# Kernel tuning notes

Hardware: AMD Instinct MI355X
Metric: run time of the kernel (lower is better)

Reference implementation:

```python
import jax, jax.numpy as jnp
import numpy as np

HID = 1024
INTER = 4096
CLIP = 2.5          # config.clip_init_val; SymQuantizer clips to [-CLIP, CLIP]
W_BITS = 8
IN_BITS = 8
EPS = 1e-12         # BertLayerNorm eps


def sym_quant(x, clip, bits):
    """BiT SymQuantizer (layerwise): clamp, scale by global max-abs, round.
    STE: grads flow only through the clamp (zero outside [-clip, clip])."""
    n = float(2 ** (bits - 1) - 1)
    xc = jnp.clip(x, -clip, clip)
    m = jax.lax.stop_gradient(jnp.max(jnp.abs(xc)))
    s = n / m
    q = jnp.round(xc * s) / s
    return xc + jax.lax.stop_gradient(q - xc)


def setup_inputs() -> dict:
    key = jax.random.key(0)
    k0, k1, k2 = jax.random.split(key, 3)
    B, S = 4, 4096
    hidden_states = jax.random.normal(k0, (B, S, INTER), jnp.float32)
    input_tensor = jax.random.normal(k1, (B, S, HID), jnp.float32)
    W = jax.random.normal(k2, (HID, INTER), jnp.float32) * (1.0 / np.sqrt(INTER))
    b = jnp.zeros((HID,), jnp.float32)
    gamma = jnp.ones((HID,), jnp.float32)
    beta = jnp.zeros((HID,), jnp.float32)
    return {"hidden_states": hidden_states, "input_tensor": input_tensor,
            "W": W, "b": b, "gamma": gamma, "beta": beta}


def reference(hidden_states, input_tensor, W, b, gamma, beta):
    # QuantizeLinear: quantize weight and activation, then F.linear
    Wq = sym_quant(W, CLIP, W_BITS)          # [HID, INTER]
    xq = sym_quant(hidden_states, CLIP, IN_BITS)  # [B, S, INTER]
    h = jnp.einsum('bsi,oi->bso', xq, Wq) + b     # [B, S, HID]
    # dropout(p=0.0 / eval mode) is identity
    y = h + input_tensor
    # BertLayerNorm, eps=1e-12
    mu = jnp.mean(y, axis=-1, keepdims=True)
    var = jnp.mean((y - mu) ** 2, axis=-1, keepdims=True)
    return gamma * (y - mu) / jnp.sqrt(var + EPS) + beta
```

## Files before the change

### kernel.cpp

```cpp
#include <hip/hip_runtime.h>
#include <stdint.h>

#define MTOT  16384
#define KDIM  4096
#define NDIM  1024
#define CLIPV 2.5f

typedef __attribute__((ext_vector_type(4)))  int i32x4;
typedef __attribute__((ext_vector_type(16))) int i32x16;
typedef __attribute__((address_space(3))) void lvoid;
typedef __attribute__((address_space(1))) void gvoid;

#define G2L16(g, l) __builtin_amdgcn_global_load_lds((gvoid*)(g), (lvoid*)(l), 16, 0, 0)

__global__ __launch_bounds__(256) void maxabs_kernel(
    const float4* __restrict__ x, int n4, unsigned* __restrict__ slot) {
  __shared__ float red[4];
  float m = 0.f;
  const int stride = gridDim.x * blockDim.x;
  for (int i = blockIdx.x * blockDim.x + threadIdx.x; i < n4; i += stride) {
    float4 v = x[i];
    m = fmaxf(m, fmaxf(fmaxf(fabsf(v.x), fabsf(v.y)),
                       fmaxf(fabsf(v.z), fabsf(v.w))));
    if (__any(m >= CLIPV)) break;
  }
  m = fminf(m, CLIPV);
#pragma unroll
  for (int off = 32; off > 0; off >>= 1) m = fmaxf(m, __shfl_xor(m, off));
  if ((threadIdx.x & 63) == 0) red[threadIdx.x >> 6] = m;
  __syncthreads();
  if (threadIdx.x == 0) {
    float bm = fmaxf(fmaxf(red[0], red[1]), fmaxf(red[2], red[3]));
    atomicMax(slot, __float_as_uint(bm));
  }
}

__global__ __launch_bounds__(256) void quant_kernel(
    const float4* __restrict__ x, unsigned* __restrict__ q, int n4,
    const unsigned* __restrict__ slot) {
  const float m = fminf(__uint_as_float(*slot), CLIPV);
  const float s = 127.0f / m;
  const int stride = gridDim.x * blockDim.x;
#pragma unroll 4
  for (int i = blockIdx.x * blockDim.x + threadIdx.x; i < n4; i += stride) {
    float4 v = x[i];
    int a = (int)rintf(fminf(fmaxf(v.x, -CLIPV), CLIPV) * s);
    int b = (int)rintf(fminf(fmaxf(v.y, -CLIPV), CLIPV) * s);
    int c = (int)rintf(fminf(fmaxf(v.z, -CLIPV), CLIPV) * s);
    int d = (int)rintf(fminf(fmaxf(v.w, -CLIPV), CLIPV) * s);
    q[i] = (unsigned)(a & 255) | ((unsigned)(b & 255) << 8) |
           ((unsigned)(c & 255) << 16) | ((unsigned)(d & 255) << 24);
  }
}

__global__ __launch_bounds__(256, 2) void gemm_i8(
    const int8_t* __restrict__ qA, const int8_t* __restrict__ qB,
    float* __restrict__ out, const unsigned* __restrict__ slot_x,
    const unsigned* __restrict__ slot_w) {
  __shared__ __align__(16) int8_t As[128 * 128];
  __shared__ __align__(16) int8_t Bs[256 * 128];

  const int t  = threadIdx.x;
  const int l  = t & 63;
  const int w  = t >> 6;
  const int wm = (w & 1) * 64;
  const int wn = (w >> 1) * 128;
  const int lr = l & 31;
  const int lh = l >> 5;

  const long m0 = (long)blockIdx.y * 128;
  const long n0 = (long)blockIdx.x * 256;

  i32x16 acc[2][4] = {};

  const int8_t* gA[4];
  const int8_t* gB[8];
#pragma unroll
  for (int j = 0; j < 4; ++j) {
    const int s = t + 256 * j, row = s >> 3, cc = (s & 7) ^ (row & 7);
    gA[j] = qA + (m0 + row) * KDIM + cc * 16;
  }
#pragma unroll
  for (int j = 0; j < 8; ++j) {
    const int s = t + 256 * j, row = s >> 3, cc = (s & 7) ^ (row & 7);
    gB[j] = qB + (n0 + row) * KDIM + cc * 16;
  }
  const int ldsb = (t & 192) * 16;

  int abase[2], amask[2], bbase[4], bmask[4];
#pragma unroll
  for (int mt = 0; mt < 2; ++mt) {
    const int ra = wm + mt * 32 + lr;
    abase[mt] = ra * 128; amask[mt] = ra & 7;
  }
#pragma unroll
  for (int nt = 0; nt < 4; ++nt) {
    const int rb = wn + nt * 32 + lr;
    bbase[nt] = rb * 128; bmask[nt] = rb & 7;
  }

  for (int k0 = 0; k0 < KDIM; k0 += 128) {
#pragma unroll
    for (int j = 0; j < 4; ++j) G2L16(gA[j] + k0, As + ldsb + j * 4096);
#pragma unroll
    for (int j = 0; j < 8; ++j) G2L16(gB[j] + k0, Bs + ldsb + j * 4096);
    __syncthreads();
#pragma unroll
    for (int kk = 0; kk < 4; ++kk) {
      const int c = kk * 2 + lh;
      i32x4 a0 = *(const i32x4*)(As + abase[0] + ((c ^ amask[0]) << 4));
      i32x4 a1 = *(const i32x4*)(As + abase[1] + ((c ^ amask[1]) << 4));
      i32x4 b0 = *(const i32x4*)(Bs + bbase[0] + ((c ^ bmask[0]) << 4));
      i32x4 b1 = *(const i32x4*)(Bs + bbase[1] + ((c ^ bmask[1]) << 4));
      i32x4 b2 = *(const i32x4*)(Bs + bbase[2] + ((c ^ bmask[2]) << 4));
      i32x4 b3 = *(const i32x4*)(Bs + bbase[3] + ((c ^ bmask[3]) << 4));
      acc[0][0] = __builtin_amdgcn_mfma_i32_32x32x32_i8(a0, b0, acc[0][0], 0, 0, 0);
      acc[1][0] = __builtin_amdgcn_mfma_i32_32x32x32_i8(a1, b0, acc[1][0], 0, 0, 0);
      acc[0][1] = __builtin_amdgcn_mfma_i32_32x32x32_i8(a0, b1, acc[0][1], 0, 0, 0);
      acc[1][1] = __builtin_amdgcn_mfma_i32_32x32x32_i8(a1, b1, acc[1][1], 0, 0, 0);
      acc[0][2] = __builtin_amdgcn_mfma_i32_32x32x32_i8(a0, b2, acc[0][2], 0, 0, 0);
      acc[1][2] = __builtin_amdgcn_mfma_i32_32x32x32_i8(a1, b2, acc[1][2], 0, 0, 0);
      acc[0][3] = __builtin_amdgcn_mfma_i32_32x32x32_i8(a0, b3, acc[0][3], 0, 0, 0);
      acc[1][3] = __builtin_amdgcn_mfma_i32_32x32x32_i8(a1, b3, acc[1][3], 0, 0, 0);
    }
    __syncthreads();
  }

  const float mx = fminf(__uint_as_float(*slot_x), CLIPV);
  const float mw = fminf(__uint_as_float(*slot_w), CLIPV);
  const float S  = mx * mw * (1.0f / (127.0f * 127.0f));

#pragma unroll
  for (int mt = 0; mt < 2; ++mt)
#pragma unroll
    for (int r = 0; r < 16; ++r) {
      const long row = m0 + wm + mt * 32 + (r & 3) + 8 * (r >> 2) + 4 * lh;
      float* orow = out + row * NDIM + n0 + wn + lr;
#pragma unroll
      for (int nt = 0; nt < 4; ++nt)
        orow[nt * 32] = (float)acc[mt][nt][r] * S;
    }
}

__global__ __launch_bounds__(256) void ln_kernel(
    float* __restrict__ h, const float* __restrict__ resid,
    const float* __restrict__ bias, const float* __restrict__ gamma,
    const float* __restrict__ beta) {
  __shared__ float red[8];
  const long row = blockIdx.x;
  const int t = threadIdx.x;
  float4* hp = (float4*)(h + row * NDIM);
  const float4* rp = (const float4*)(resid + row * NDIM);
  float4 y  = hp[t];
  float4 rv = rp[t];
  float4 bv = ((const float4*)bias)[t];
  y.x += rv.x + bv.x; y.y += rv.y + bv.y; y.z += rv.z + bv.z; y.w += rv.w + bv.w;
  float sum = y.x + y.y + y.z + y.w;
  float ss  = y.x * y.x + y.y * y.y + y.z * y.z + y.w * y.w;
#pragma unroll
  for (int off = 32; off > 0; off >>= 1) {
    sum += __shfl_xor(sum, off);
    ss  += __shfl_xor(ss, off);
  }
  if ((t & 63) == 0) { red[(t >> 6) * 2] = sum; red[(t >> 6) * 2 + 1] = ss; }
  __syncthreads();
  sum = red[0] + red[2] + red[4] + red[6];
  ss  = red[1] + red[3] + red[5] + red[7];
  const float mu   = sum * (1.0f / NDIM);
  const float var  = ss * (1.0f / NDIM) - mu * mu;
  const float rstd = rsqrtf(var + 1e-12f);
  float4 g  = ((const float4*)gamma)[t];
  float4 be = ((const float4*)beta)[t];
  float4 o;
  o.x = g.x * (y.x - mu) * rstd + be.x;
  o.y = g.y * (y.y - mu) * rstd + be.y;
  o.z = g.z * (y.z - mu) * rstd + be.z;
  o.w = g.w * (y.w - mu) * rstd + be.w;
  hp[t] = o;
}

extern "C" void kernel_launch(void* const* d_in, const int* in_sizes, int n_in,
                              void* d_out, int out_size, void* d_ws,
                              size_t ws_size, hipStream_t stream) {
  const float* x     = (const float*)d_in[0];
  const float* resid = (const float*)d_in[1];
  const float* W     = (const float*)d_in[2];
  const float* b     = (const float*)d_in[3];
  const float* gamma = (const float*)d_in[4];
  const float* beta  = (const float*)d_in[5];
  float* out = (float*)d_out;

  int8_t* qA = (int8_t*)d_ws;
  int8_t* qW = qA + (size_t)MTOT * KDIM;
  unsigned* slots = (unsigned*)(qW + (size_t)NDIM * KDIM);

  hipMemsetAsync(slots, 0, 8, stream);
  maxabs_kernel<<<2048, 256, 0, stream>>>((const float4*)x, MTOT * KDIM / 4, slots);
  maxabs_kernel<<<512, 256, 0, stream>>>((const float4*)W, NDIM * KDIM / 4, slots + 1);
  quant_kernel<<<2048, 256, 0, stream>>>((const float4*)x, (unsigned*)qA,
                                         MTOT * KDIM / 4, slots);
  quant_kernel<<<512, 256, 0, stream>>>((const float4*)W, (unsigned*)qW,
                                        NDIM * KDIM / 4, slots + 1);
  gemm_i8<<<dim3(NDIM / 256, MTOT / 128), 256, 0, stream>>>(qA, qW, out, slots,
                                                            slots + 1);
  ln_kernel<<<MTOT, 256, 0, stream>>>(out, resid, b, gamma, beta);
}
```

Measured before the change: 566.9 us.

## Double-buffer int8 GEMM, fuse bias+residual into epilogue, wave-per-row LayerNorm

The GEMM K-loop moves from a single 128-wide LDS tile to a double-buffered 64-wide tile, so the next tile's global-to-LDS loads overlap the MFMAs on the current one, using explicit waitcnt and barriers. Bias and residual addition move into the GEMM epilogue, so the LayerNorm kernel no longer reads the residual. LayerNorm now gives one wavefront per row and drops the shared-memory reduction. The quantize kernel writes 16 bytes per thread instead of 4. The risks are the hand-written vmcnt counts and the change to the swizzle pattern.

```diff
diff --git a/kernel.cpp b/kernel.cpp
--- a/kernel.cpp
+++ b/kernel.cpp
@@ -5,6 +5,8 @@
 #define KDIM  4096
 #define NDIM  1024
 #define CLIPV 2.5f
+#define BK    64
+#define NSTEP (KDIM / BK)
 
 typedef __attribute__((ext_vector_type(4)))  int i32x4;
 typedef __attribute__((ext_vector_type(16))) int i32x16;
@@ -36,29 +38,36 @@
 }
 
 __global__ __launch_bounds__(256) void quant_kernel(
-    const float4* __restrict__ x, unsigned* __restrict__ q, int n4,
+    const float4* __restrict__ x, uint4* __restrict__ q, int n16,
     const unsigned* __restrict__ slot) {
   const float m = fminf(__uint_as_float(*slot), CLIPV);
   const float s = 127.0f / m;
   const int stride = gridDim.x * blockDim.x;
-#pragma unroll 4
-  for (int i = blockIdx.x * blockDim.x + threadIdx.x; i < n4; i += stride) {
-    float4 v = x[i];
-    int a = (int)rintf(fminf(fmaxf(v.x, -CLIPV), CLIPV) * s);
-    int b = (int)rintf(fminf(fmaxf(v.y, -CLIPV), CLIPV) * s);
-    int c = (int)rintf(fminf(fmaxf(v.z, -CLIPV), CLIPV) * s);
-    int d = (int)rintf(fminf(fmaxf(v.w, -CLIPV), CLIPV) * s);
-    q[i] = (unsigned)(a & 255) | ((unsigned)(b & 255) << 8) |
-           ((unsigned)(c & 255) << 16) | ((unsigned)(d & 255) << 24);
+  for (int i = blockIdx.x * blockDim.x + threadIdx.x; i < n16; i += stride) {
+    const float4* xp = x + 4 * (long)i;
+    uint4 o;
+    unsigned* op = (unsigned*)&o;
+#pragma unroll
+    for (int j = 0; j < 4; ++j) {
+      float4 v = xp[j];
+      int a = (int)rintf(fminf(fmaxf(v.x, -CLIPV), CLIPV) * s);
+      int b = (int)rintf(fminf(fmaxf(v.y, -CLIPV), CLIPV) * s);
+      int c = (int)rintf(fminf(fmaxf(v.z, -CLIPV), CLIPV) * s);
+      int d = (int)rintf(fminf(fmaxf(v.w, -CLIPV), CLIPV) * s);
+      op[j] = (unsigned)(a & 255) | ((unsigned)(b & 255) << 8) |
+              ((unsigned)(c & 255) << 16) | ((unsigned)(d & 255) << 24);
+    }
+    q[i] = o;
   }
 }
 
 __global__ __launch_bounds__(256, 2) void gemm_i8(
     const int8_t* __restrict__ qA, const int8_t* __restrict__ qB,
-    float* __restrict__ out, const unsigned* __restrict__ slot_x,
-    const unsigned* __restrict__ slot_w) {
-  __shared__ __align__(16) int8_t As[128 * 128];
-  __shared__ __align__(16) int8_t Bs[256 * 128];
+    float* __restrict__ out, const float* __restrict__ resid,
+    const float* __restrict__ bias,
+    const unsigned* __restrict__ slot_x, const unsigned* __restrict__ slot_w) {
+  __shared__ __align__(16) int8_t As[2][128 * BK];
+  __shared__ __align__(16) int8_t Bs[2][256 * BK];
 
   const int t  = threadIdx.x;
   const int l  = t & 63;
@@ -73,16 +82,16 @@
 
   i32x16 acc[2][4] = {};
 
-  const int8_t* gA[4];
-  const int8_t* gB[8];
+  const int8_t* gA[2];
+  const int8_t* gB[4];
+#pragma unroll
+  for (int j = 0; j < 2; ++j) {
+    const int s = t + 256 * j, row = s >> 2, cc = (s & 3) ^ ((row >> 1) & 3);
+    gA[j] = qA + (m0 + row) * KDIM + cc * 16;
+  }
 #pragma unroll
   for (int j = 0; j < 4; ++j) {
-    const int s = t + 256 * j, row = s >> 3, cc = (s & 7) ^ (row & 7);
-    gA[j] = qA + (m0 + row) * KDIM + cc * 16;
-  }
-#pragma unroll
-  for (int j = 0; j < 8; ++j) {
-    const int s = t + 256 * j, row = s >> 3, cc = (s & 7) ^ (row & 7);
+    const int s = t + 256 * j, row = s >> 2, cc = (s & 3) ^ ((row >> 1) & 3);
     gB[j] = qB + (n0 + row) * KDIM + cc * 16;
   }
   const int ldsb = (t & 192) * 16;
@@ -91,29 +100,49 @@
 #pragma unroll
   for (int mt = 0; mt < 2; ++mt) {
     const int ra = wm + mt * 32 + lr;
-    abase[mt] = ra * 128; amask[mt] = ra & 7;
+    abase[mt] = ra * BK; amask[mt] = (ra >> 1) & 3;
   }
 #pragma unroll
   for (int nt = 0; nt < 4; ++nt) {
     const int rb = wn + nt * 32 + lr;
-    bbase[nt] = rb * 128; bmask[nt] = rb & 7;
-  }
-
-  for (int k0 = 0; k0 < KDIM; k0 += 128) {
-#pragma unroll
-    for (int j = 0; j < 4; ++j) G2L16(gA[j] + k0, As + ldsb + j * 4096);
-#pragma unroll
-    for (int j = 0; j < 8; ++j) G2L16(gB[j] + k0, Bs + ldsb + j * 4096);
-    __syncthreads();
-#pragma unroll
-    for (int kk = 0; kk < 4; ++kk) {
+    bbase[nt] = rb * BK; bmask[nt] = (rb >> 1) & 3;
+  }
+
+#define STAGE(buf, koff)                                      \
+  do {                                                        \
+    _Pragma("unroll")                                         \
+    for (int j = 0; j < 2; ++j)                               \
+      G2L16(gA[j] + (koff), &As[buf][ldsb + j * 4096]);       \
+    _Pragma("unroll")                                         \
+    for (int j = 0; j < 4; ++j)                               \
+      G2L16(gB[j] + (koff), &Bs[buf][ldsb + j * 4096]);       \
+  } while (0)
+
+  STAGE(0, 0);
+
+#pragma unroll 2
+  for (int ks = 0; ks < NSTEP; ++ks) {
+    const int cur = ks & 1;
+    if (ks + 1 < NSTEP) {
+      STAGE(cur ^ 1, (ks + 1) * BK);
+      asm volatile("s_waitcnt vmcnt(6)" ::: "memory");
+    } else {
+      asm volatile("s_waitcnt vmcnt(0)" ::: "memory");
+    }
+    __builtin_amdgcn_s_barrier();
+    asm volatile("" ::: "memory");
+
+    const int8_t* A_ = As[cur];
+    const int8_t* B_ = Bs[cur];
+#pragma unroll
+    for (int kk = 0; kk < 2; ++kk) {
       const int c = kk * 2 + lh;
-      i32x4 a0 = *(const i32x4*)(As + abase[0] + ((c ^ amask[0]) << 4));
-      i32x4 a1 = *(const i32x4*)(As + abase[1] + ((c ^ amask[1]) << 4));
-      i32x4 b0 = *(const i32x4*)(Bs + bbase[0] + ((c ^ bmask[0]) << 4));
-      i32x4 b1 = *(const i32x4*)(Bs + bbase[1] + ((c ^ bmask[1]) << 4));
-      i32x4 b2 = *(const i32x4*)(Bs + bbase[2] + ((c ^ bmask[2]) << 4));
-      i32x4 b3 = *(const i32x4*)(Bs + bbase[3] + ((c ^ bmask[3]) << 4));
+      i32x4 a0 = *(const i32x4*)(A_ + abase[0] + ((c ^ amask[0]) << 4));
+      i32x4 a1 = *(const i32x4*)(A_ + abase[1] + ((c ^ amask[1]) << 4));
+      i32x4 b0 = *(const i32x4*)(B_ + bbase[0] + ((c ^ bmask[0]) << 4));
+      i32x4 b1 = *(const i32x4*)(B_ + bbase[1] + ((c ^ bmask[1]) << 4));
+      i32x4 b2 = *(const i32x4*)(B_ + bbase[2] + ((c ^ bmask[2]) << 4));
+      i32x4 b3 = *(const i32x4*)(B_ + bbase[3] + ((c ^ bmask[3]) << 4));
       acc[0][0] = __builtin_amdgcn_mfma_i32_32x32x32_i8(a0, b0, acc[0][0], 0, 0, 0);
       acc[1][0] = __builtin_amdgcn_mfma_i32_32x32x32_i8(a1, b0, acc[1][0], 0, 0, 0);
       acc[0][1] = __builtin_amdgcn_mfma_i32_32x32x32_i8(a0, b1, acc[0][1], 0, 0, 0);
@@ -123,60 +152,67 @@
       acc[0][3] = __builtin_amdgcn_mfma_i32_32x32x32_i8(a0, b3, acc[0][3], 0, 0, 0);
       acc[1][3] = __builtin_amdgcn_mfma_i32_32x32x32_i8(a1, b3, acc[1][3], 0, 0, 0);
     }
-    __syncthreads();
-  }
+    asm volatile("s_waitcnt lgkmcnt(0)" ::: "memory");
+    __builtin_amdgcn_s_barrier();
+    asm volatile("" ::: "memory");
+  }
+#undef STAGE
 
   const float mx = fminf(__uint_as_float(*slot_x), CLIPV);
   const float mw = fminf(__uint_as_float(*slot_w), CLIPV);
   const float S  = mx * mw * (1.0f / (127.0f * 127.0f));
 
+  const int coln = (int)n0 + wn + lr;
+  float bv[4];
+#pragma unroll
+  for (int nt = 0; nt < 4; ++nt) bv[nt] = bias[coln + nt * 32];
+
 #pragma unroll
   for (int mt = 0; mt < 2; ++mt)
 #pragma unroll
     for (int r = 0; r < 16; ++r) {
       const long row = m0 + wm + mt * 32 + (r & 3) + 8 * (r >> 2) + 4 * lh;
-      float* orow = out + row * NDIM + n0 + wn + lr;
+      float* orow = out + row * NDIM + coln;
+      const float* rrow = resid + row * NDIM + coln;
 #pragma unroll
       for (int nt = 0; nt < 4; ++nt)
-        orow[nt * 32] = (float)acc[mt][nt][r] * S;
+        orow[nt * 32] = (float)acc[mt][nt][r] * S + bv[nt] + rrow[nt * 32];
     }
 }
 
 __global__ __launch_bounds__(256) void ln_kernel(
-    float* __restrict__ h, const float* __restrict__ resid,
-    const float* __restrict__ bias, const float* __restrict__ gamma,
+    float* __restrict__ h, const float* __restrict__ gamma,
     const float* __restrict__ beta) {
-  __shared__ float red[8];
-  const long row = blockIdx.x;
-  const int t = threadIdx.x;
+  const int lane = threadIdx.x & 63;
+  const long row = (long)blockIdx.x * 4 + (threadIdx.x >> 6);
   float4* hp = (float4*)(h + row * NDIM);
-  const float4* rp = (const float4*)(resid + row * NDIM);
-  float4 y  = hp[t];
-  float4 rv = rp[t];
-  float4 bv = ((const float4*)bias)[t];
-  y.x += rv.x + bv.x; y.y += rv.y + bv.y; y.z += rv.z + bv.z; y.w += rv.w + bv.w;
-  float sum = y.x + y.y + y.z + y.w;
-  float ss  = y.x * y.x + y.y * y.y + y.z * y.z + y.w * y.w;
+  float4 y[4];
+  float sum = 0.f, ss = 0.f;
+#pragma unroll
+  for (int j = 0; j < 4; ++j) {
+    y[j] = hp[lane + 64 * j];
+    sum += y[j].x + y[j].y + y[j].z + y[j].w;
+    ss  += y[j].x * y[j].x + y[j].y * y[j].y + y[j].z * y[j].z + y[j].w * y[j].w;
+  }
 #pragma unroll
   for (int off = 32; off > 0; off >>= 1) {
     sum += __shfl_xor(sum, off);
     ss  += __shfl_xor(ss, off);
   }
-  if ((t & 63) == 0) { red[(t >> 6) * 2] = sum; red[(t >> 6) * 2 + 1] = ss; }
-  __syncthreads();
-  sum = red[0] + red[2] + red[4] + red[6];
-  ss  = red[1] + red[3] + red[5] + red[7];
   const float mu   = sum * (1.0f / NDIM);
   const float var  = ss * (1.0f / NDIM) - mu * mu;
   const float rstd = rsqrtf(var + 1e-12f);
-  float4 g  = ((const float4*)gamma)[t];
-  float4 be = ((const float4*)beta)[t];
-  float4 o;
-  o.x = g.x * (y.x - mu) * rstd + be.x;
-  o.y = g.y * (y.y - mu) * rstd + be.y;
-  o.z = g.z * (y.z - mu) * rstd + be.z;
-  o.w = g.w * (y.w - mu) * rstd + be.w;
-  hp[t] = o;
+#pragma unroll
+  for (int j = 0; j < 4; ++j) {
+    float4 g  = ((const float4*)gamma)[lane + 64 * j];
+    float4 be = ((const float4*)beta)[lane + 64 * j];
+    float4 o;
+    o.x = g.x * (y[j].x - mu) * rstd + be.x;
+    o.y = g.y * (y[j].y - mu) * rstd + be.y;
+    o.z = g.z * (y[j].z - mu) * rstd + be.z;
+    o.w = g.w * (y[j].w - mu) * rstd + be.w;
+    hp[lane + 64 * j] = o;
+  }
 }
 
 extern "C" void kernel_launch(void* const* d_in, const int* in_sizes, int n_in,
@@ -197,11 +233,11 @@
   hipMemsetAsync(slots, 0, 8, stream);
   maxabs_kernel<<<2048, 256, 0, stream>>>((const float4*)x, MTOT * KDIM / 4, slots);
   maxabs_kernel<<<512, 256, 0, stream>>>((const float4*)W, NDIM * KDIM / 4, slots + 1);
-  quant_kernel<<<2048, 256, 0, stream>>>((const float4*)x, (unsigned*)qA,
-                                         MTOT * KDIM / 4, slots);
-  quant_kernel<<<512, 256, 0, stream>>>((const float4*)W, (unsigned*)qW,
-                                        NDIM * KDIM / 4, slots + 1);
-  gemm_i8<<<dim3(NDIM / 256, MTOT / 128), 256, 0, stream>>>(qA, qW, out, slots,
-                                                            slots + 1);
-  ln_kernel<<<MTOT, 256, 0, stream>>>(out, resid, b, gamma, beta);
-}
+  quant_kernel<<<2048, 256, 0, stream>>>((const float4*)x, (uint4*)qA,
+                                         MTOT * KDIM / 16, slots);
+  quant_kernel<<<512, 256, 0, stream>>>((const float4*)W, (uint4*)qW,
+                                        NDIM * KDIM / 16, slots + 1);
+  gemm_i8<<<dim3(NDIM / 256, MTOT / 128), 256, 0, stream>>>(qA, qW, out, resid, b,
+                                                            slots, slots + 1);
+  ln_kernel<<<MTOT / 4, 256, 0, stream>>>(out, gamma, beta);
+}
```

Measured after the change: 572.2 us. About the same (+0.9%).
